# Kernel tuning notes

Measured on AMD Instinct MI355X. Metric: run time of the kernel, lower is better.

Reference implementation:

```python
import jax, jax.numpy as jnp
import numpy as np

# LIF / LI constants (norse defaults, model='super', alpha=100, dt=1e-3)
DT = 1e-3
TAU_SYN_INV = 200.0
TAU_MEM_INV = 100.0
V_TH = 1.0
ALPHA = 100.0

@jax.custom_vjp
def spike(x):
    return (x > 0).astype(x.dtype)

def _spike_fwd(x):
    return spike(x), x

def _spike_bwd(x, g):
    # SuperSpike surrogate gradient
    return (g / (ALPHA * jnp.abs(x) + 1.0) ** 2,)

spike.defvjp(_spike_fwd, _spike_bwd)

def conv2d(x, w, b):
    y = jax.lax.conv_general_dilated(x, w, window_strides=(1, 1), padding='VALID',
                                     dimension_numbers=('NCHW', 'OIHW', 'NCHW'))
    return y + b[None, :, None, None]

def maxpool2(x):
    return jax.lax.reduce_window(x, -jnp.inf, jax.lax.max,
                                 (1, 1, 2, 2), (1, 1, 2, 2), 'VALID')

def lif_step(inp, v, i):
    # feed-forward LIF: decay v and i, spike, reset, then inject input current
    v_dec = v + DT * TAU_MEM_INV * (-v + i)
    i_dec = i * (1.0 - DT * TAU_SYN_INV)
    z = spike(v_dec - V_TH)
    v_new = (1.0 - z) * v_dec  # v_reset = 0
    i_new = i_dec + inp
    return z, v_new, i_new

def setup_inputs() -> dict:
    key = jax.random.key(0)
    ks = jax.random.split(key, 8)
    T, B = 64, 256
    x = jax.random.normal(ks[0], (T, B, 1, 28, 28), jnp.float32)
    w1 = jax.random.normal(ks[1], (20, 1, 5, 5), jnp.float32) * 0.2
    b1 = jax.random.normal(ks[2], (20,), jnp.float32) * 0.05
    w2 = jax.random.normal(ks[3], (50, 20, 5, 5), jnp.float32) * 0.045
    b2 = jax.random.normal(ks[4], (50,), jnp.float32) * 0.02
    w_fc = jax.random.normal(ks[5], (500, 800), jnp.float32) * 0.035
    b_fc = jax.random.normal(ks[6], (500,), jnp.float32) * 0.02
    w_out = jax.random.normal(ks[7], (10, 500), jnp.float32) * 0.045
    return {"x": x, "w1": w1, "b1": b1, "w2": w2, "b2": b2,
            "w_fc": w_fc, "b_fc": b_fc, "w_out": w_out}

def reference(x, w1, b1, w2, b2, w_fc, b_fc, w_out):
    T, B = x.shape[0], x.shape[1]
    dtype = x.dtype
    s0 = (jnp.zeros((B, 20, 24, 24), dtype), jnp.zeros((B, 20, 24, 24), dtype))
    s1 = (jnp.zeros((B, 50, 8, 8), dtype), jnp.zeros((B, 50, 8, 8), dtype))
    s2 = (jnp.zeros((B, 500), dtype), jnp.zeros((B, 500), dtype))
    so = (jnp.zeros((B, 10), dtype), jnp.zeros((B, 10), dtype))

    def step(carry, xt):
        (v0, i0), (v1, i1), (v2, i2), (vo, io) = carry
        z = conv2d(xt, w1, b1)                 # [B,20,24,24]
        z, v0, i0 = lif_step(z, v0, i0)
        z = maxpool2(z)                        # [B,20,12,12]
        z = 10.0 * conv2d(z, w2, b2)           # [B,50,8,8]
        z, v1, i1 = lif_step(z, v1, i1)
        z = maxpool2(z)                        # [B,50,4,4]
        z = z.reshape(B, -1)                   # [B,800]
        z = z @ w_fc.T + b_fc                  # [B,500]
        z, v2, i2 = lif_step(z, v2, i2)
        # LI output cell (no spiking): decay then inject linear input
        v_new = vo + DT * TAU_MEM_INV * (-vo + io)
        i_dec = io * (1.0 - DT * TAU_SYN_INV)
        i_new = i_dec + jax.nn.relu(z) @ w_out.T
        return ((v0, i0), (v1, i1), (v2, i2), (v_new, i_new)), v_new

    _, voltages = jax.lax.scan(step, (s0, s1, s2, so), x)
    return voltages  # [T,B,10]
```

## Files before the change

kernel.cpp:

```cpp
#include <hip/hip_runtime.h>
#include <cstdint>
#include <cstddef>


#define TSTEPS 64
#define NB 256

#define RFL(v) __builtin_amdgcn_readfirstlane(v)

__global__ __launch_bounds__(256)
void transpose_wfc(const float* __restrict__ wfc, float* __restrict__ wfcT) {
    int idx = blockIdx.x * 256 + threadIdx.x;
    if (idx < 500 * 800) {
        int o = idx / 800, j = idx % 800;
        wfcT[j * 500 + o] = wfc[idx];
    }
}

__global__ __launch_bounds__(512, 2)
void snn_forward(const float* __restrict__ x,
                 const float* __restrict__ w1,
                 const float* __restrict__ b1,
                 const float* __restrict__ w2,
                 const float* __restrict__ b2,
                 const float* __restrict__ fcw,
                 long fc_sj, long fc_so,
                 const float* __restrict__ bfc,
                 const float* __restrict__ wout,
                 float* __restrict__ out)
{
    const float CM = 0.1f;
    const float CS = 0.8f;

    const int b   = blockIdx.x;
    const int tid = threadIdx.x;

    __shared__ float xs[2][28 * 36];
    __shared__ float p1[20 * 12 * 12];
    __shared__ float w1L[500];
    __shared__ float woutL[5000];
    __shared__ unsigned int bm2[25];
    __shared__ unsigned int bm3[16];
    __shared__ int list2i[816];
    __shared__ unsigned short list3s[512];
    __shared__ int nn2s, nn3s;

    if (tid < 500) w1L[tid] = w1[tid];
    if (tid < 25)  bm2[tid] = 0u;
    for (int i = tid; i < 5000; i += 512) woutL[i] = wout[i];

    const int sr0 = tid / 28,         sc0_ = tid - sr0 * 28;
    const int has2 = (tid + 512) < 784;
    const int sr1 = (tid + 512) / 28, sc1_ = (tid + 512) - sr1 * 28;

    {
        const float* xp = x + ((size_t)b) * 784;
        xs[0][sr0 * 36 + sc0_] = xp[tid];
        if (has2) xs[0][sr1 * 36 + sc1_] = xp[tid + 512];
    }

    const int l1  = (tid < 480);
    const int c   = tid / 24;
    const int sub = tid % 24;
    const int pr  = sub >> 1;
    const int chh = sub & 1;
    const int r0  = pr * 2;
    const int c0  = chh * 12;

    float v0a[12], v0b[12], i0a[12], i0b[12];
    #pragma unroll
    for (int j = 0; j < 12; ++j) { v0a[j] = 0.f; v0b[j] = 0.f; i0a[j] = 0.f; i0b[j] = 0.f; }

    const int l2  = (tid < 400);
    const int oc2 = tid >> 3;
    const int y2  = tid & 7;
    const float bias2 = l2 ? b2[oc2] : 0.f;
    const float bias1 = l1 ? b1[c] : 0.f;
    const float* w2base = w2 + (size_t)oc2 * 500;

    float vL2[8], iL2[8];
    #pragma unroll
    for (int q = 0; q < 8; ++q) { vL2[q] = 0.f; iL2[q] = 0.f; }

    float vL3 = 0.f, iL3 = 0.f;
    const float bfc_r = (tid < 500) ? bfc[tid] : 0.f;

    float vO = 0.f, iO = 0.f;

    const char* __restrict__ fcb = (const char*)fcw;
    const int coff = (int)((long)tid * fc_so) * 4;

    __syncthreads();

    for (int ts = 0; ts < TSTEPS; ++ts) {
        const int cur = ts & 1, nxt = cur ^ 1;

        float xpre0 = 0.f, xpre1 = 0.f;
        if (ts + 1 < TSTEPS) {
            const float* xpn = x + ((size_t)(ts + 1) * NB + b) * 784;
            xpre0 = xpn[tid];
            if (has2) xpre1 = xpn[tid + 512];
        }

        float wcur[25];
        if (l2) {
            #pragma unroll
            for (int q = 0; q < 25; ++q) wcur[q] = w2base[q];
        }

        if (l1) {
            float acc0[12], acc1[12];
            #pragma unroll
            for (int j = 0; j < 12; ++j) { acc0[j] = 0.f; acc1[j] = 0.f; }
            float wc[5], wp[5];
            #pragma unroll
            for (int ir = 0; ir < 6; ++ir) {
                float xr[16];
                const float4* rp = (const float4*)(xs[cur] + (r0 + ir) * 36 + c0);
                #pragma unroll
                for (int q = 0; q < 4; ++q) {
                    float4 f = rp[q];
                    xr[4*q+0] = f.x; xr[4*q+1] = f.y; xr[4*q+2] = f.z; xr[4*q+3] = f.w;
                }
                if (ir < 5) {
                    #pragma unroll
                    for (int k = 0; k < 5; ++k) wc[k] = w1L[c * 25 + ir * 5 + k];
                    #pragma unroll
                    for (int kc = 0; kc < 5; ++kc) {
                        const float w = wc[kc];
                        #pragma unroll
                        for (int j = 0; j < 12; ++j)
                            acc0[j] = __fmaf_rn(w, xr[j + kc], acc0[j]);
                    }
                }
                if (ir >= 1) {
                    #pragma unroll
                    for (int kc = 0; kc < 5; ++kc) {
                        const float w = wp[kc];
                        #pragma unroll
                        for (int j = 0; j < 12; ++j)
                            acc1[j] = __fmaf_rn(w, xr[j + kc], acc1[j]);
                    }
                }
                #pragma unroll
                for (int k = 0; k < 5; ++k) wp[k] = wc[k];
            }
            unsigned int zb0 = 0, zb1 = 0;
            #pragma unroll
            for (int j = 0; j < 12; ++j) {
                const float inp = __fadd_rn(acc0[j], bias1);
                const float vd  = __fadd_rn(v0a[j], __fmul_rn(CM, __fsub_rn(i0a[j], v0a[j])));
                const float id  = __fmul_rn(i0a[j], CS);
                const int z = (__fsub_rn(vd, 1.0f) > 0.0f);
                v0a[j] = z ? 0.f : vd;
                i0a[j] = __fadd_rn(id, inp);
                zb0 |= (unsigned)z << j;
            }
            #pragma unroll
            for (int j = 0; j < 12; ++j) {
                const float inp = __fadd_rn(acc1[j], bias1);
                const float vd  = __fadd_rn(v0b[j], __fmul_rn(CM, __fsub_rn(i0b[j], v0b[j])));
                const float id  = __fmul_rn(i0b[j], CS);
                const int z = (__fsub_rn(vd, 1.0f) > 0.0f);
                v0b[j] = z ? 0.f : vd;
                i0b[j] = __fadd_rn(id, inp);
                zb1 |= (unsigned)z << j;
            }
            const unsigned int zp = zb0 | zb1;
            #pragma unroll
            for (int jj = 0; jj < 6; ++jj)
                p1[(c * 12 + pr) * 12 + chh * 6 + jj] = ((zp >> (2 * jj)) & 3u) ? 1.0f : 0.0f;
        }
        if (ts + 1 < TSTEPS) {
            xs[nxt][sr0 * 36 + sc0_] = xpre0;
            if (has2) xs[nxt][sr1 * 36 + sc1_] = xpre1;
        }
        __syncthreads();

        if (l2) {
            float acc[8];
            #pragma unroll
            for (int xx = 0; xx < 8; ++xx) acc[xx] = 0.f;

            float4 ra, rb, rc;
            {
                const float4* pp = (const float4*)(p1 + y2 * 12);
                ra = pp[0]; rb = pp[1]; rc = pp[2];
            }
            float wnxt[25];

            for (int ic = 0; ic < 20; ++ic) {
                if (ic + 1 < 20) {
                    #pragma unroll
                    for (int q = 0; q < 25; ++q) wnxt[q] = w2base[(ic + 1) * 25 + q];
                }
                #pragma unroll
                for (int kr = 0; kr < 5; ++kr) {
                    float4 na, nb, nc;
                    const bool last = (ic == 19) && (kr == 4);
                    if (!last) {
                        const int nic = (kr == 4) ? ic + 1 : ic;
                        const int nkr = (kr == 4) ? 0 : kr + 1;
                        const float4* pp = (const float4*)(p1 + (nic * 12 + y2 + nkr) * 12);
                        na = pp[0]; nb = pp[1]; nc = pp[2];
                    }
                    const float pv[12] = { ra.x,ra.y,ra.z,ra.w, rb.x,rb.y,rb.z,rb.w, rc.x,rc.y,rc.z,rc.w };
                    const float w0  = wcur[kr*5+0], w1_ = wcur[kr*5+1], w2_ = wcur[kr*5+2];
                    const float w3_ = wcur[kr*5+3], w4_ = wcur[kr*5+4];
                    #pragma unroll
                    for (int xx = 0; xx < 8; ++xx) acc[xx] = __fmaf_rn(w0, pv[xx],     acc[xx]);
                    #pragma unroll
                    for (int xx = 0; xx < 8; ++xx) acc[xx] = __fmaf_rn(w1_, pv[xx + 1], acc[xx]);
                    #pragma unroll
                    for (int xx = 0; xx < 8; ++xx) acc[xx] = __fmaf_rn(w2_, pv[xx + 2], acc[xx]);
                    #pragma unroll
                    for (int xx = 0; xx < 8; ++xx) acc[xx] = __fmaf_rn(w3_, pv[xx + 3], acc[xx]);
                    #pragma unroll
                    for (int xx = 0; xx < 8; ++xx) acc[xx] = __fmaf_rn(w4_, pv[xx + 4], acc[xx]);
                    if (!last) { ra = na; rb = nb; rc = nc; }
                }
                if (ic + 1 < 20) {
                    #pragma unroll
                    for (int q = 0; q < 25; ++q) wcur[q] = wnxt[q];
                }
            }

            unsigned int pb = 0;
            const unsigned int bitbase = (unsigned)((oc2 & 1) * 16 + (y2 >> 1) * 4);
            #pragma unroll
            for (int xx = 0; xx < 8; ++xx) {
                const float inp = __fmul_rn(10.0f, __fadd_rn(acc[xx], bias2));
                const float vd  = __fadd_rn(vL2[xx], __fmul_rn(CM, __fsub_rn(iL2[xx], vL2[xx])));
                const float id  = __fmul_rn(iL2[xx], CS);
                const int z = (__fsub_rn(vd, 1.0f) > 0.0f);
                vL2[xx] = z ? 0.f : vd;
                iL2[xx] = __fadd_rn(id, inp);
                if (z) pb |= 1u << (bitbase + (xx >> 1));
            }
            if (pb) atomicOr(&bm2[oc2 >> 1], pb);
        }
        __syncthreads();

        if (tid < 64) {
            unsigned int bits = (tid < 25) ? bm2[tid] : 0u;
            if (tid < 25) bm2[tid] = 0u;
            int cnt = __popc(bits);
            int inc = cnt;
            #pragma unroll
            for (int d = 1; d < 32; d <<= 1) {
                int n = __shfl_up(inc, d);
                if (tid >= d) inc += n;
            }
            int off = inc - cnt;
            if (tid == 24) nn2s = inc;
            const int jstride = (int)fc_sj * 4;
            const int base = tid * 32;
            while (bits) {
                const int bb = __builtin_ctz(bits);
                bits &= bits - 1;
                list2i[off++] = (base + bb) * jstride;
            }
        }
        __syncthreads();

        if (tid < 500) {
            const int nn2 = nn2s;
            float acc = 0.f;
            int k = 0;

#define FC_LOAD32(dst, kk) do { _Pragma("unroll") \
            for (int q_ = 0; q_ < 32; ++q_) { \
                const int o_ = RFL(list2i[(kk) + q_]); \
                dst[q_] = *(const float*)(fcb + (size_t)(unsigned)(o_ + coff)); } } while (0)
#define FC_FMA32(src) do { _Pragma("unroll") \
            for (int q_ = 0; q_ < 32; ++q_) acc = __fmaf_rn(1.0f, src[q_], acc); } while (0)

            const int nb32 = nn2 >> 5;
            if (nb32 >= 1) {
                float A[32], B[32];
                FC_LOAD32(A, 0);
                int j = 1;
                for (; j + 1 < nb32; j += 2) {
                    FC_LOAD32(B, j * 32);
                    FC_FMA32(A);
                    FC_LOAD32(A, (j + 1) * 32);
                    FC_FMA32(B);
                }
                if (j < nb32) {
                    FC_LOAD32(B, j * 32);
                    FC_FMA32(A);
                    FC_FMA32(B);
                } else {
                    FC_FMA32(A);
                }
                k = nb32 * 32;
            }
            {
                const int rem = nn2 - k;
                float t[31];
                #pragma unroll
                for (int q = 0; q < 31; ++q) {
                    if (q < rem) {
                        const int o_ = RFL(list2i[k + q]);
                        t[q] = *(const float*)(fcb + (size_t)(unsigned)(o_ + coff));
                    } else t[q] = 0.f;
                }
                #pragma unroll
                for (int q = 0; q < 31; ++q)
                    if (q < rem) acc = __fmaf_rn(1.0f, t[q], acc);
            }
#undef FC_LOAD32
#undef FC_FMA32

            const float inp = __fadd_rn(acc, bfc_r);
            const float vd  = __fadd_rn(vL3, __fmul_rn(CM, __fsub_rn(iL3, vL3)));
            const float id  = __fmul_rn(iL3, CS);
            const int z = (__fsub_rn(vd, 1.0f) > 0.0f);
            vL3 = z ? 0.f : vd;
            iL3 = __fadd_rn(id, inp);
            const unsigned long long m = __ballot(z);
            if ((tid & 63) == 0) {
                bm3[(tid >> 5)]     = (unsigned int)m;
                bm3[(tid >> 5) + 1] = (unsigned int)(m >> 32);
            }
        }
        __syncthreads();

        if (tid < 64) {
            unsigned int bits = (tid < 16) ? bm3[tid] : 0u;
            int cnt = __popc(bits);
            int inc = cnt;
            #pragma unroll
            for (int d = 1; d < 16; d <<= 1) {
                int n = __shfl_up(inc, d);
                if (tid >= d) inc += n;
            }
            int off = inc - cnt;
            if (tid == 15) nn3s = inc;
            while (bits) {
                const int bb = __builtin_ctz(bits);
                bits &= bits - 1;
                list3s[off++] = (unsigned short)(tid * 32 + bb);
            }
        }
        __syncthreads();

        {
            const int otid = tid - 500;
            if (otid >= 0 && otid < 10) {
                const float* wrow_ = woutL + otid * 500;
                const int nn3 = nn3s;
                float acc = 0.f;
                int k = 0;
                const int kfull = nn3 & ~7;
                if (kfull > 0) {
                    float a[8];
                    #pragma unroll
                    for (int q = 0; q < 8; ++q)
                        a[q] = wrow_[list3s[q]];
                    for (k = 8; k < kfull; k += 8) {
                        float bv[8];
                        #pragma unroll
                        for (int q = 0; q < 8; ++q)
                            bv[q] = wrow_[list3s[k + q]];
                        #pragma unroll
                        for (int q = 0; q < 8; ++q)
                            acc = __fmaf_rn(1.0f, a[q], acc);
                        #pragma unroll
                        for (int q = 0; q < 8; ++q)
                            a[q] = bv[q];
                    }
                    #pragma unroll
                    for (int q = 0; q < 8; ++q)
                        acc = __fmaf_rn(1.0f, a[q], acc);
                    k = kfull;
                }
                {
                    const int rem = nn3 - k;
                    float t[7];
                    #pragma unroll
                    for (int q = 0; q < 7; ++q)
                        t[q] = (q < rem) ? wrow_[list3s[k + q]] : 0.f;
                    #pragma unroll
                    for (int q = 0; q < 7; ++q)
                        if (q < rem) acc = __fmaf_rn(1.0f, t[q], acc);
                }
                const float vn = __fadd_rn(vO, __fmul_rn(CM, __fsub_rn(iO, vO)));
                iO = __fadd_rn(__fmul_rn(iO, CS), acc);
                vO = vn;
                out[((size_t)ts * NB + b) * 10 + otid] = vn;
            }
        }
    }
}

extern "C" void kernel_launch(void* const* d_in, const int* in_sizes, int n_in,
                              void* d_out, int out_size, void* d_ws, size_t ws_size,
                              hipStream_t stream)
{
    const float* x    = (const float*)d_in[0];
    const float* w1   = (const float*)d_in[1];
    const float* b1   = (const float*)d_in[2];
    const float* w2   = (const float*)d_in[3];
    const float* b2   = (const float*)d_in[4];
    const float* wfc  = (const float*)d_in[5];
    const float* bfc  = (const float*)d_in[6];
    const float* wout = (const float*)d_in[7];
    float* out = (float*)d_out;

    const float* fcptr = wfc;
    long sj = 1, so = 800;
    if (ws_size >= (size_t)500 * 800 * sizeof(float)) {
        float* wfcT = (float*)d_ws;
        transpose_wfc<<<(500 * 800 + 255) / 256, 256, 0, stream>>>(wfc, wfcT);
        fcptr = wfcT; sj = 500; so = 1;
    }

    snn_forward<<<NB, 512, 0, stream>>>(x, w1, b1, w2, b2, fcptr, sj, so, bfc, wout, out);
}
```

Baseline: 1.589 ms.

## Software-pipeline FC and output layers one timestep behind conv2 stage

Restructures the per-timestep schedule so the sparse FC gather for step t-1 runs interleaved with the conv2 loop of step t. FC weight loads are issued in chunks of 24 per input channel iteration, which hides global-memory latency behind conv2 FMAs. The layer-3 spike compaction moves into the same phase as the layer-2 compaction, and the output layer also runs one step behind, which removes two block-wide barriers per timestep. An epilogue drains the last step. The cost is extra register pressure and padding of the spike list with zero offsets.

```diff
diff --git a/kernel.cpp b/kernel.cpp
--- a/kernel.cpp
+++ b/kernel.cpp
@@ -41,12 +41,13 @@
     __shared__ float woutL[5000];
     __shared__ unsigned int bm2[25];
     __shared__ unsigned int bm3[16];
-    __shared__ int list2i[816];
+    __shared__ int list2i[848];
     __shared__ unsigned short list3s[512];
     __shared__ int nn2s, nn3s;
 
     if (tid < 500) w1L[tid] = w1[tid];
     if (tid < 25)  bm2[tid] = 0u;
+    if (tid == 0)  { nn2s = 0; nn3s = 0; }
     for (int i = tid; i < 5000; i += 512) woutL[i] = wout[i];
 
     const int sr0 = tid / 28,         sc0_ = tid - sr0 * 28;
@@ -88,7 +89,18 @@
     float vO = 0.f, iO = 0.f;
 
     const char* __restrict__ fcb = (const char*)fcw;
-    const int coff = (int)((long)tid * fc_so) * 4;
+    const int coff  = (int)((long)tid * fc_so) * 4;
+    const int coffE = (tid < 500) ? coff : 0;
+
+#define FC_ISSUE24(F_, kk_) do { _Pragma("unroll") \
+    for (int q_ = 0; q_ < 24; ++q_) { \
+        const int o_ = RFL(list2i[(kk_) + q_]); \
+        F_[q_] = *(const float*)(fcb + (size_t)(unsigned)(o_ + coffE)); } } while (0)
+#define FC_CONSUME24(fca_, F_, kk_, nlim_) do { _Pragma("unroll") \
+    for (int q_ = 0; q_ < 24; ++q_) { \
+        const float m_ = (((kk_) + q_) < (nlim_)) ? 1.0f : 0.0f; \
+        (fca_) = __fmaf_rn(m_, F_[q_], (fca_)); } \
+    (kk_) += 24; } while (0)
 
     __syncthreads();
 
@@ -101,7 +113,6 @@
             xpre0 = xpn[tid];
             if (has2) xpre1 = xpn[tid + 512];
         }
-
         float wcur[25];
         if (l2) {
             #pragma unroll
@@ -177,67 +188,98 @@
         }
         __syncthreads();
 
-        if (l2) {
+        {
+            const int nlim = (ts > 0) ? nn2s : 0;
+            float fca = 0.f;
+            int kk = 0;
+
             float acc[8];
-            #pragma unroll
-            for (int xx = 0; xx < 8; ++xx) acc[xx] = 0.f;
-
             float4 ra, rb, rc;
-            {
+            float wnxt[25];
+            if (l2) {
+                #pragma unroll
+                for (int xx = 0; xx < 8; ++xx) acc[xx] = 0.f;
                 const float4* pp = (const float4*)(p1 + y2 * 12);
                 ra = pp[0]; rb = pp[1]; rc = pp[2];
             }
-            float wnxt[25];
 
             for (int ic = 0; ic < 20; ++ic) {
-                if (ic + 1 < 20) {
-                    #pragma unroll
-                    for (int q = 0; q < 25; ++q) wnxt[q] = w2base[(ic + 1) * 25 + q];
-                }
-                #pragma unroll
-                for (int kr = 0; kr < 5; ++kr) {
-                    float4 na, nb, nc;
-                    const bool last = (ic == 19) && (kr == 4);
-                    if (!last) {
-                        const int nic = (kr == 4) ? ic + 1 : ic;
-                        const int nkr = (kr == 4) ? 0 : kr + 1;
-                        const float4* pp = (const float4*)(p1 + (nic * 12 + y2 + nkr) * 12);
-                        na = pp[0]; nb = pp[1]; nc = pp[2];
-                    }
-                    const float pv[12] = { ra.x,ra.y,ra.z,ra.w, rb.x,rb.y,rb.z,rb.w, rc.x,rc.y,rc.z,rc.w };
-                    const float w0  = wcur[kr*5+0], w1_ = wcur[kr*5+1], w2_ = wcur[kr*5+2];
-                    const float w3_ = wcur[kr*5+3], w4_ = wcur[kr*5+4];
-                    #pragma unroll
-                    for (int xx = 0; xx < 8; ++xx) acc[xx] = __fmaf_rn(w0, pv[xx],     acc[xx]);
-                    #pragma unroll
-                    for (int xx = 0; xx < 8; ++xx) acc[xx] = __fmaf_rn(w1_, pv[xx + 1], acc[xx]);
-                    #pragma unroll
-                    for (int xx = 0; xx < 8; ++xx) acc[xx] = __fmaf_rn(w2_, pv[xx + 2], acc[xx]);
-                    #pragma unroll
-                    for (int xx = 0; xx < 8; ++xx) acc[xx] = __fmaf_rn(w3_, pv[xx + 3], acc[xx]);
-                    #pragma unroll
-                    for (int xx = 0; xx < 8; ++xx) acc[xx] = __fmaf_rn(w4_, pv[xx + 4], acc[xx]);
-                    if (!last) { ra = na; rb = nb; rc = nc; }
-                }
-                if (ic + 1 < 20) {
-                    #pragma unroll
-                    for (int q = 0; q < 25; ++q) wcur[q] = wnxt[q];
-                }
-            }
-
-            unsigned int pb = 0;
-            const unsigned int bitbase = (unsigned)((oc2 & 1) * 16 + (y2 >> 1) * 4);
-            #pragma unroll
-            for (int xx = 0; xx < 8; ++xx) {
-                const float inp = __fmul_rn(10.0f, __fadd_rn(acc[xx], bias2));
-                const float vd  = __fadd_rn(vL2[xx], __fmul_rn(CM, __fsub_rn(iL2[xx], vL2[xx])));
-                const float id  = __fmul_rn(iL2[xx], CS);
+                float F[24];
+                const bool doB = (kk < nlim);
+                if (doB) FC_ISSUE24(F, kk);
+
+                if (l2) {
+                    if (ic + 1 < 20) {
+                        #pragma unroll
+                        for (int q = 0; q < 25; ++q) wnxt[q] = w2base[(ic + 1) * 25 + q];
+                    }
+                    #pragma unroll
+                    for (int kr = 0; kr < 5; ++kr) {
+                        float4 na, nb, nc;
+                        const bool last = (ic == 19) && (kr == 4);
+                        if (!last) {
+                            const int nic = (kr == 4) ? ic + 1 : ic;
+                            const int nkr = (kr == 4) ? 0 : kr + 1;
+                            const float4* pp = (const float4*)(p1 + (nic * 12 + y2 + nkr) * 12);
+                            na = pp[0]; nb = pp[1]; nc = pp[2];
+                        }
+                        const float pv[12] = { ra.x,ra.y,ra.z,ra.w, rb.x,rb.y,rb.z,rb.w, rc.x,rc.y,rc.z,rc.w };
+                        const float w0  = wcur[kr*5+0], w1_ = wcur[kr*5+1], w2_ = wcur[kr*5+2];
+                        const float w3_ = wcur[kr*5+3], w4_ = wcur[kr*5+4];
+                        #pragma unroll
+                        for (int xx = 0; xx < 8; ++xx) acc[xx] = __fmaf_rn(w0, pv[xx],     acc[xx]);
+                        #pragma unroll
+                        for (int xx = 0; xx < 8; ++xx) acc[xx] = __fmaf_rn(w1_, pv[xx + 1], acc[xx]);
+                        #pragma unroll
+                        for (int xx = 0; xx < 8; ++xx) acc[xx] = __fmaf_rn(w2_, pv[xx + 2], acc[xx]);
+                        #pragma unroll
+                        for (int xx = 0; xx < 8; ++xx) acc[xx] = __fmaf_rn(w3_, pv[xx + 3], acc[xx]);
+                        #pragma unroll
+                        for (int xx = 0; xx < 8; ++xx) acc[xx] = __fmaf_rn(w4_, pv[xx + 4], acc[xx]);
+                        if (!last) { ra = na; rb = nb; rc = nc; }
+                    }
+                    if (ic + 1 < 20) {
+                        #pragma unroll
+                        for (int q = 0; q < 25; ++q) wcur[q] = wnxt[q];
+                    }
+                }
+
+                if (doB) FC_CONSUME24(fca, F, kk, nlim);
+            }
+            while (kk < nlim) {
+                float F2[24];
+                FC_ISSUE24(F2, kk);
+                FC_CONSUME24(fca, F2, kk, nlim);
+            }
+
+            if (l2) {
+                unsigned int pb = 0;
+                const unsigned int bitbase = (unsigned)((oc2 & 1) * 16 + (y2 >> 1) * 4);
+                #pragma unroll
+                for (int xx = 0; xx < 8; ++xx) {
+                    const float inp = __fmul_rn(10.0f, __fadd_rn(acc[xx], bias2));
+                    const float vd  = __fadd_rn(vL2[xx], __fmul_rn(CM, __fsub_rn(iL2[xx], vL2[xx])));
+                    const float id  = __fmul_rn(iL2[xx], CS);
+                    const int z = (__fsub_rn(vd, 1.0f) > 0.0f);
+                    vL2[xx] = z ? 0.f : vd;
+                    iL2[xx] = __fadd_rn(id, inp);
+                    if (z) pb |= 1u << (bitbase + (xx >> 1));
+                }
+                if (pb) atomicOr(&bm2[oc2 >> 1], pb);
+            }
+            if (ts > 0 && tid < 500) {
+                const float inp = __fadd_rn(fca, bfc_r);
+                const float vd  = __fadd_rn(vL3, __fmul_rn(CM, __fsub_rn(iL3, vL3)));
+                const float id  = __fmul_rn(iL3, CS);
                 const int z = (__fsub_rn(vd, 1.0f) > 0.0f);
-                vL2[xx] = z ? 0.f : vd;
-                iL2[xx] = __fadd_rn(id, inp);
-                if (z) pb |= 1u << (bitbase + (xx >> 1));
-            }
-            if (pb) atomicOr(&bm2[oc2 >> 1], pb);
+                vL3 = z ? 0.f : vd;
+                iL3 = __fadd_rn(id, inp);
+                const unsigned long long m = __ballot(z);
+                if ((tid & 63) == 0) {
+                    bm3[(tid >> 5)]     = (unsigned int)m;
+                    bm3[(tid >> 5) + 1] = (unsigned int)(m >> 32);
+                }
+            }
         }
         __syncthreads();
 
@@ -253,6 +295,7 @@
             }
             int off = inc - cnt;
             if (tid == 24) nn2s = inc;
+            const int tot = __shfl(inc, 24);
             const int jstride = (int)fc_sj * 4;
             const int base = tid * 32;
             while (bits) {
@@ -260,59 +303,79 @@
                 bits &= bits - 1;
                 list2i[off++] = (base + bb) * jstride;
             }
+            if (tid >= 32) list2i[tot + (tid - 32)] = 0;
+        } else if (tid < 128 && ts > 0) {
+            const int t3 = tid - 64;
+            unsigned int bits = (t3 < 16) ? bm3[t3] : 0u;
+            int cnt = __popc(bits);
+            int inc = cnt;
+            #pragma unroll
+            for (int d = 1; d < 16; d <<= 1) {
+                int n = __shfl_up(inc, d);
+                if (t3 >= d) inc += n;
+            }
+            int off = inc - cnt;
+            if (t3 == 15) nn3s = inc;
+            while (bits) {
+                const int bb = __builtin_ctz(bits);
+                bits &= bits - 1;
+                list3s[off++] = (unsigned short)(t3 * 32 + bb);
+            }
         }
         __syncthreads();
 
+        if (ts > 0) {
+            const int otid = tid - 500;
+            if (otid >= 0 && otid < 10) {
+                const float* wrow_ = woutL + otid * 500;
+                const int nn3 = nn3s;
+                float acc = 0.f;
+                int k = 0;
+                const int kfull = nn3 & ~7;
+                if (kfull > 0) {
+                    float a[8];
+                    #pragma unroll
+                    for (int q = 0; q < 8; ++q) a[q] = wrow_[list3s[q]];
+                    for (k = 8; k < kfull; k += 8) {
+                        float bv[8];
+                        #pragma unroll
+                        for (int q = 0; q < 8; ++q) bv[q] = wrow_[list3s[k + q]];
+                        #pragma unroll
+                        for (int q = 0; q < 8; ++q) acc = __fmaf_rn(1.0f, a[q], acc);
+                        #pragma unroll
+                        for (int q = 0; q < 8; ++q) a[q] = bv[q];
+                    }
+                    #pragma unroll
+                    for (int q = 0; q < 8; ++q) acc = __fmaf_rn(1.0f, a[q], acc);
+                    k = kfull;
+                }
+                {
+                    const int rem = nn3 - k;
+                    float t[7];
+                    #pragma unroll
+                    for (int q = 0; q < 7; ++q) t[q] = (q < rem) ? wrow_[list3s[k + q]] : 0.f;
+                    #pragma unroll
+                    for (int q = 0; q < 7; ++q) if (q < rem) acc = __fmaf_rn(1.0f, t[q], acc);
+                }
+                const float vn = __fadd_rn(vO, __fmul_rn(CM, __fsub_rn(iO, vO)));
+                iO = __fadd_rn(__fmul_rn(iO, CS), acc);
+                vO = vn;
+                out[((size_t)(ts - 1) * NB + b) * 10 + otid] = vn;
+            }
+        }
+    }
+
+    {
+        const int nlim = nn2s;
+        float fca = 0.f;
+        int kk = 0;
+        while (kk < nlim) {
+            float F[24];
+            FC_ISSUE24(F, kk);
+            FC_CONSUME24(fca, F, kk, nlim);
+        }
         if (tid < 500) {
-            const int nn2 = nn2s;
-            float acc = 0.f;
-            int k = 0;
-
-#define FC_LOAD32(dst, kk) do { _Pragma("unroll") \
-            for (int q_ = 0; q_ < 32; ++q_) { \
-                const int o_ = RFL(list2i[(kk) + q_]); \
-                dst[q_] = *(const float*)(fcb + (size_t)(unsigned)(o_ + coff)); } } while (0)
-#define FC_FMA32(src) do { _Pragma("unroll") \
-            for (int q_ = 0; q_ < 32; ++q_) acc = __fmaf_rn(1.0f, src[q_], acc); } while (0)
-
-            const int nb32 = nn2 >> 5;
-            if (nb32 >= 1) {
-                float A[32], B[32];
-                FC_LOAD32(A, 0);
-                int j = 1;
-                for (; j + 1 < nb32; j += 2) {
-                    FC_LOAD32(B, j * 32);
-                    FC_FMA32(A);
-                    FC_LOAD32(A, (j + 1) * 32);
-                    FC_FMA32(B);
-                }
-                if (j < nb32) {
-                    FC_LOAD32(B, j * 32);
-                    FC_FMA32(A);
-                    FC_FMA32(B);
-                } else {
-                    FC_FMA32(A);
-                }
-                k = nb32 * 32;
-            }
-            {
-                const int rem = nn2 - k;
-                float t[31];
-                #pragma unroll
-                for (int q = 0; q < 31; ++q) {
-                    if (q < rem) {
-                        const int o_ = RFL(list2i[k + q]);
-                        t[q] = *(const float*)(fcb + (size_t)(unsigned)(o_ + coff));
-                    } else t[q] = 0.f;
-                }
-                #pragma unroll
-                for (int q = 0; q < 31; ++q)
-                    if (q < rem) acc = __fmaf_rn(1.0f, t[q], acc);
-            }
-#undef FC_LOAD32
-#undef FC_FMA32
-
-            const float inp = __fadd_rn(acc, bfc_r);
+            const float inp = __fadd_rn(fca, bfc_r);
             const float vd  = __fadd_rn(vL3, __fmul_rn(CM, __fsub_rn(iL3, vL3)));
             const float id  = __fmul_rn(iL3, CS);
             const int z = (__fsub_rn(vd, 1.0f) > 0.0f);
@@ -324,72 +387,63 @@
                 bm3[(tid >> 5) + 1] = (unsigned int)(m >> 32);
             }
         }
-        __syncthreads();
-
-        if (tid < 64) {
-            unsigned int bits = (tid < 16) ? bm3[tid] : 0u;
-            int cnt = __popc(bits);
-            int inc = cnt;
-            #pragma unroll
-            for (int d = 1; d < 16; d <<= 1) {
-                int n = __shfl_up(inc, d);
-                if (tid >= d) inc += n;
-            }
-            int off = inc - cnt;
-            if (tid == 15) nn3s = inc;
-            while (bits) {
-                const int bb = __builtin_ctz(bits);
-                bits &= bits - 1;
-                list3s[off++] = (unsigned short)(tid * 32 + bb);
-            }
-        }
-        __syncthreads();
-
-        {
-            const int otid = tid - 500;
-            if (otid >= 0 && otid < 10) {
-                const float* wrow_ = woutL + otid * 500;
-                const int nn3 = nn3s;
-                float acc = 0.f;
-                int k = 0;
-                const int kfull = nn3 & ~7;
-                if (kfull > 0) {
-                    float a[8];
-                    #pragma unroll
-                    for (int q = 0; q < 8; ++q)
-                        a[q] = wrow_[list3s[q]];
-                    for (k = 8; k < kfull; k += 8) {
-                        float bv[8];
-                        #pragma unroll
-                        for (int q = 0; q < 8; ++q)
-                            bv[q] = wrow_[list3s[k + q]];
-                        #pragma unroll
-                        for (int q = 0; q < 8; ++q)
-                            acc = __fmaf_rn(1.0f, a[q], acc);
-                        #pragma unroll
-                        for (int q = 0; q < 8; ++q)
-                            a[q] = bv[q];
-                    }
-                    #pragma unroll
-                    for (int q = 0; q < 8; ++q)
-                        acc = __fmaf_rn(1.0f, a[q], acc);
-                    k = kfull;
-                }
-                {
-                    const int rem = nn3 - k;
-                    float t[7];
-                    #pragma unroll
-                    for (int q = 0; q < 7; ++q)
-                        t[q] = (q < rem) ? wrow_[list3s[k + q]] : 0.f;
-                    #pragma unroll
-                    for (int q = 0; q < 7; ++q)
-                        if (q < rem) acc = __fmaf_rn(1.0f, t[q], acc);
-                }
-                const float vn = __fadd_rn(vO, __fmul_rn(CM, __fsub_rn(iO, vO)));
-                iO = __fadd_rn(__fmul_rn(iO, CS), acc);
-                vO = vn;
-                out[((size_t)ts * NB + b) * 10 + otid] = vn;
-            }
+    }
+    __syncthreads();
+    if (tid < 64) {
+        unsigned int bits = (tid < 16) ? bm3[tid] : 0u;
+        int cnt = __popc(bits);
+        int inc = cnt;
+        #pragma unroll
+        for (int d = 1; d < 16; d <<= 1) {
+            int n = __shfl_up(inc, d);
+            if (tid >= d) inc += n;
+        }
+        int off = inc - cnt;
+        if (tid == 15) nn3s = inc;
+        while (bits) {
+            const int bb = __builtin_ctz(bits);
+            bits &= bits - 1;
+            list3s[off++] = (unsigned short)(tid * 32 + bb);
+        }
+    }
+    __syncthreads();
+    {
+        const int otid = tid - 500;
+        if (otid >= 0 && otid < 10) {
+            const float* wrow_ = woutL + otid * 500;
+            const int nn3 = nn3s;
+            float acc = 0.f;
+            int k = 0;
+            const int kfull = nn3 & ~7;
+            if (kfull > 0) {
+                float a[8];
+                #pragma unroll
+                for (int q = 0; q < 8; ++q) a[q] = wrow_[list3s[q]];
+                for (k = 8; k < kfull; k += 8) {
+                    float bv[8];
+                    #pragma unroll
+                    for (int q = 0; q < 8; ++q) bv[q] = wrow_[list3s[k + q]];
+                    #pragma unroll
+                    for (int q = 0; q < 8; ++q) acc = __fmaf_rn(1.0f, a[q], acc);
+                    #pragma unroll
+                    for (int q = 0; q < 8; ++q) a[q] = bv[q];
+                }
+                #pragma unroll
+                for (int q = 0; q < 8; ++q) acc = __fmaf_rn(1.0f, a[q], acc);
+                k = kfull;
+            }
+            {
+                const int rem = nn3 - k;
+                float t[7];
+                #pragma unroll
+                for (int q = 0; q < 7; ++q) t[q] = (q < rem) ? wrow_[list3s[k + q]] : 0.f;
+                #pragma unroll
+                for (int q = 0; q < 7; ++q) if (q < rem) acc = __fmaf_rn(1.0f, t[q], acc);
+            }
+            const float vn = __fadd_rn(vO, __fmul_rn(CM, __fsub_rn(iO, vO)));
+            iO = __fadd_rn(__fmul_rn(iO, CS), acc);
+            vO = vn;
+            out[((size_t)(TSTEPS - 1) * NB + b) * 10 + otid] = vn;
         }
     }
 }
```

Result: slower. 2.513 ms (+58.2%).
